# Optimization experiments

Measured on AMD Instinct MI355X. Metric: run time of the kernel, lower is better.

## Reference

```python
import jax, jax.numpy as jnp
import numpy as np

EMB_SCALE = 0.001  # embedding_scale when normalize=False


def setup_inputs() -> dict:
    key = jax.random.key(0)
    k1, k2 = jax.random.split(key)
    N, S, C, V, K = 8, 4096, 2, 128, 512
    x0 = jax.random.normal(k1, (N, S, C, V), dtype=jnp.float32)
    embedding = jax.random.normal(k2, (C, K, V), dtype=jnp.float32) * EMB_SCALE
    return {"x0": x0, "embedding": embedding}


def reference(x0, embedding):
    # normalize=False path: x = x0, embedding used as-is
    N, S, C, V = x0.shape
    K = embedding.shape[1]
    x = x0
    xf = x.reshape(N * S, C, V)  # (B, C, V), B = N*S tokens

    # (the ||x||^2 term is constant over k). Avoids materializing (B, C, K, V).
    dots = jnp.einsum('bcv,ckv->bck', xf, embedding)          # (B, C, K)
    e_sq = jnp.sum(embedding * embedding, axis=2)             # (C, K)
    dist2 = e_sq[None, :, :] - 2.0 * dots                     # (B, C, K)
    index = jnp.argmin(dist2, axis=2)                         # (B, C) int

    # Entropy of codebook usage (original divides by len(index) == B rows)
    B = N * S
    hist = jnp.bincount(index.reshape(-1), length=K).astype(jnp.float32)
    prob = hist / jnp.float32(B)
    entropy = -jnp.sum(jnp.where(hist > 0, prob * jnp.log(jnp.maximum(prob, 1e-30)), 0.0))

    # Gather: output[b, c] = embedding[c, index[b, c]]
    output = embedding[jnp.arange(C), index]                  # (B, C, V)
    output = output.reshape(N, S, C, V)

    out0 = jax.lax.stop_gradient(output - x) + x              # straight-through
    out1 = jnp.sum((jax.lax.stop_gradient(x) - output) ** 2, axis=3)  # (N,S,C)
    out2 = (jnp.sum((x - jax.lax.stop_gradient(output)) ** 2, axis=3)
            + jnp.sum((x - x0) ** 2, axis=3))                 # (N,S,C); (x-x0)==0 here
    return (out0, out1, out2, entropy)
```

## Files before the change

### kernel.cpp

```cpp
#include <hip/hip_runtime.h>
#include <math.h>

#define N_TOK    32768
#define C_CH     2
#define V_DIM    128
#define K_CODES  512
#define TPB      64
#define CAND_CAP 768
#define BAND     4.0e-3f

typedef short     bf16v8 __attribute__((ext_vector_type(8)));
typedef float     f32x4  __attribute__((ext_vector_type(4)));
typedef unsigned  u32x4  __attribute__((ext_vector_type(4)));

__device__ inline unsigned f2bf(float f) {
    unsigned u = __float_as_uint(f);
    return (u + 0x7FFFu + ((u >> 16) & 1u)) >> 16;
}
__device__ inline unsigned mapf(float d) {
    unsigned u = __float_as_uint(d);
    return ((int)u < 0) ? ~u : (u | 0x80000000u);
}
__device__ inline float unmapf(unsigned u) {
    return __uint_as_float((u & 0x80000000u) ? (u & 0x7FFFFFFFu) : ~u);
}

__global__ __launch_bounds__(64) void vq_prep(const float* __restrict__ emb,
                                              float* __restrict__ e_sq,
                                              unsigned int* __restrict__ hist,
                                              unsigned char* __restrict__ img) {
    const int row  = blockIdx.x;
    const int lane = threadIdx.x;
    const float a = emb[(size_t)row * V_DIM + lane];
    const float b = emb[(size_t)row * V_DIM + 64 + lane];
    float s = a * a + b * b;
#pragma unroll
    for (int off = 32; off; off >>= 1) s += __shfl_down(s, off);
    if (lane == 0) {
        e_sq[row] = s;
        if (row < K_CODES) hist[row] = 0u;
    }
    if (lane < 16) {
        const float* src = emb + (size_t)row * V_DIM + lane * 8;
        u32x4 val;
#pragma unroll
        for (int q = 0; q < 4; ++q)
            val[q] = f2bf(src[2 * q]) | (f2bf(src[2 * q + 1]) << 16);
        *reinterpret_cast<u32x4*>(img + ((size_t)row * 16 + lane) * 16) = val;
    }
}

__global__ __launch_bounds__(256, 2) void vq_main(const float* __restrict__ x0,
                                                  const float* __restrict__ emb,
                                                  const float* __restrict__ e_sq,
                                                  const unsigned char* __restrict__ img,
                                                  unsigned short* __restrict__ idx16,
                                                  float* __restrict__ out0,
                                                  float* __restrict__ out1,
                                                  float* __restrict__ out2) {
    __shared__ float xx_s[TPB];
    __shared__ unsigned int dmin_s[TPB];
    __shared__ unsigned long long best_s[TPB];
    __shared__ unsigned int cand[CAND_CAP];
    __shared__ int cand_n;

    const int c    = blockIdx.y;
    const int gt0  = blockIdx.x * TPB;
    const int t    = threadIdx.x;
    const int lane = t & 63;
    const int w    = t >> 6;
    const int l15  = lane & 15;
    const int l4   = lane >> 4;

    if (t < TPB) { dmin_s[t] = 0xFFFFFFFFu; best_s[t] = ~0ull; }
    if (t == 0) cand_n = 0;

    u32x4 Bf[8][4];
    {
        const unsigned char* imgc = img + (size_t)(c * K_CODES + w * 128) * 256;
#pragma unroll
        for (int ct = 0; ct < 8; ++ct)
#pragma unroll
            for (int kk = 0; kk < 4; ++kk)
                Bf[ct][kk] = *reinterpret_cast<const u32x4*>(
                    imgc + (size_t)(ct * 16 + l15) * 256 + (kk * 4 + l4) * 16);
    }
    float esq_r[8];
#pragma unroll
    for (int ct = 0; ct < 8; ++ct)
        esq_r[ct] = e_sq[c * K_CODES + w * 128 + ct * 16 + l15];

    __syncthreads();

    f32x4 raw[8];
    auto LOADX = [&](int tile_) {
        const float* xp = x0 + ((size_t)(gt0 + tile_ * 16 + l15) * C_CH + c) * V_DIM
                        + l4 * 8;
#pragma unroll
        for (int kk = 0; kk < 4; ++kk) {
            raw[2 * kk]     = *reinterpret_cast<const f32x4*>(xp + kk * 32);
            raw[2 * kk + 1] = *reinterpret_cast<const f32x4*>(xp + kk * 32 + 4);
        }
    };

    LOADX(0);
#pragma unroll
    for (int tile = 0; tile < 4; ++tile) {
        u32x4 A[4];
        float part = 0.f;
#pragma unroll
        for (int kk = 0; kk < 4; ++kk) {
            const f32x4 lo = raw[2 * kk], hi = raw[2 * kk + 1];
            u32x4 v;
            v[0] = f2bf(lo[0]) | (f2bf(lo[1]) << 16);
            v[1] = f2bf(lo[2]) | (f2bf(lo[3]) << 16);
            v[2] = f2bf(hi[0]) | (f2bf(hi[1]) << 16);
            v[3] = f2bf(hi[2]) | (f2bf(hi[3]) << 16);
            A[kk] = v;
#pragma unroll
            for (int z = 0; z < 4; ++z) {
                part = fmaf(lo[z], lo[z], part);
                part = fmaf(hi[z], hi[z], part);
            }
        }
        part += __shfl_xor(part, 16);
        part += __shfl_xor(part, 32);
        if (w == 0 && l4 == 0) xx_s[tile * 16 + l15] = part;

        if (tile < 3) LOADX(tile + 1);

        f32x4 acc[8];
#pragma unroll
        for (int ct = 0; ct < 8; ++ct) acc[ct] = (f32x4){0.f, 0.f, 0.f, 0.f};
#pragma unroll
        for (int kk = 0; kk < 4; ++kk)
#pragma unroll
            for (int ct = 0; ct < 8; ++ct)
                acc[ct] = __builtin_amdgcn_mfma_f32_16x16x32_bf16(
                    __builtin_bit_cast(bf16v8, A[kk]),
                    __builtin_bit_cast(bf16v8, Bf[ct][kk]), acc[ct], 0, 0, 0);

#pragma unroll
        for (int ct = 0; ct < 8; ++ct)
#pragma unroll
            for (int r = 0; r < 4; ++r)
                acc[ct][r] = fmaf(-2.f, acc[ct][r], esq_r[ct]);
#pragma unroll
        for (int r = 0; r < 4; ++r) {
            float v = acc[0][r];
#pragma unroll
            for (int ct = 1; ct < 8; ++ct) v = fminf(v, acc[ct][r]);
#pragma unroll
            for (int s = 1; s < 16; s <<= 1) v = fminf(v, __shfl_xor(v, s));
            if (l15 == 0)
                atomicMin(&dmin_s[tile * 16 + l4 * 4 + r], mapf(v));
        }
        __syncthreads();

#pragma unroll
        for (int r = 0; r < 4; ++r) {
            const int tok = tile * 16 + l4 * 4 + r;
            const float thr = unmapf(dmin_s[tok]) + BAND;
#pragma unroll
            for (int ct = 0; ct < 8; ++ct) {
                if (acc[ct][r] <= thr) {
                    const int k = w * 128 + ct * 16 + l15;
                    const int pos = atomicAdd(&cand_n, 1);
                    if (pos < CAND_CAP)
                        cand[pos] = ((unsigned)tok << 9) | (unsigned)k;
                }
            }
        }
    }
    __syncthreads();

    {
        const int nc = cand_n < CAND_CAP ? cand_n : CAND_CAP;
        const int g  = t >> 4;
        const int gl = t & 15;
        for (int i = g; i < nc; i += 16) {
            const unsigned key = cand[i];
            const int tok = key >> 9;
            const int kc  = key & (K_CODES - 1);
            const float* xg = x0 + ((size_t)(gt0 + tok) * C_CH + c) * V_DIM + gl * 8;
            const float* eg = emb + ((size_t)c * K_CODES + kc) * V_DIM + gl * 8;
            const f32x4 xa = *reinterpret_cast<const f32x4*>(xg);
            const f32x4 xb = *reinterpret_cast<const f32x4*>(xg + 4);
            const f32x4 ea = *reinterpret_cast<const f32x4*>(eg);
            const f32x4 eb = *reinterpret_cast<const f32x4*>(eg + 4);
            float d8 = 0.f;
#pragma unroll
            for (int z = 0; z < 4; ++z) {
                d8 = fmaf(xa[z], ea[z], d8);
                d8 = fmaf(xb[z], eb[z], d8);
            }
#pragma unroll
            for (int s = 1; s < 16; s <<= 1) d8 += __shfl_xor(d8, s);
            if (gl == 0) {
                const float d = fmaf(-2.f, d8, e_sq[c * K_CODES + kc]);
                atomicMin(&best_s[tok],
                          ((unsigned long long)mapf(d) << 32) | (unsigned)kc);
            }
        }
    }
    __syncthreads();

    if (t < TPB) {
        const unsigned long long b = best_s[t];
        const int k = (int)(b & (unsigned)(K_CODES - 1));
        const float d = unmapf((unsigned)(b >> 32));
        const float o12 = xx_s[t] + d;
        const size_t oi = (size_t)(gt0 + t) * C_CH + c;
        out1[oi] = o12;
        out2[oi] = o12;
        idx16[oi] = (unsigned short)k;
    }

#pragma unroll
    for (int p = 0; p < 8; ++p) {
        const int tok = p * 8 + (t >> 5);
        const int v4  = t & 31;
        const int k   = (int)(best_s[tok] & (unsigned long long)(K_CODES - 1));
        const f32x4 ev = *reinterpret_cast<const f32x4*>(
            emb + ((size_t)c * K_CODES + k) * V_DIM + v4 * 4);
        const f32x4 xv = *reinterpret_cast<const f32x4*>(
            x0 + ((size_t)(gt0 + tok) * C_CH + c) * V_DIM + v4 * 4);
        f32x4 ov;
#pragma unroll
        for (int z = 0; z < 4; ++z) ov[z] = (ev[z] - xv[z]) + xv[z];
        *reinterpret_cast<f32x4*>(
            out0 + ((size_t)(gt0 + tok) * C_CH + c) * V_DIM + v4 * 4) = ov;
    }
}

__global__ __launch_bounds__(256) void vq_hist(const unsigned short* __restrict__ idx16,
                                               unsigned int* __restrict__ hist) {
    __shared__ unsigned int h[K_CODES];
    const int t = threadIdx.x;
    h[t] = 0u; h[t + 256] = 0u;
    __syncthreads();
    const int base = blockIdx.x * 4096;
#pragma unroll
    for (int j = 0; j < 16; ++j)
        atomicAdd(&h[idx16[base + j * 256 + t]], 1u);
    __syncthreads();
    if (h[t])       atomicAdd(&hist[t],       h[t]);
    if (h[t + 256]) atomicAdd(&hist[t + 256], h[t + 256]);
}

__global__ __launch_bounds__(512) void vq_entropy(const unsigned int* __restrict__ hist,
                                                  float* __restrict__ ent) {
    const int t = threadIdx.x;
    float v = 0.f;
    const unsigned int h = hist[t];
    if (h > 0u) {
        const float p = (float)h * (1.0f / 32768.0f);
        v = p * logf(p);
    }
#pragma unroll
    for (int off = 32; off; off >>= 1) v += __shfl_down(v, off);
    __shared__ float s[8];
    if ((t & 63) == 0) s[t >> 6] = v;
    __syncthreads();
    if (t == 0) {
        float tot = 0.f;
#pragma unroll
        for (int i = 0; i < 8; ++i) tot += s[i];
        ent[0] = -tot;
    }
}

extern "C" void kernel_launch(void* const* d_in, const int* in_sizes, int n_in,
                              void* d_out, int out_size, void* d_ws, size_t ws_size,
                              hipStream_t stream) {
    const float* x0  = (const float*)d_in[0];
    const float* emb = (const float*)d_in[1];

    float*          e_sq  = (float*)d_ws;
    unsigned int*   hist  = (unsigned int*)((char*)d_ws + 4096);
    unsigned char*  img   = (unsigned char*)d_ws + 8192;
    unsigned short* idx16 = (unsigned short*)((char*)d_ws + 8192 + 262144);

    float* out0 = (float*)d_out;
    float* out1 = out0 + (size_t)N_TOK * C_CH * V_DIM;
    float* out2 = out1 + (size_t)N_TOK * C_CH;
    float* ent  = out2 + (size_t)N_TOK * C_CH;

    vq_prep<<<C_CH * K_CODES, 64, 0, stream>>>(emb, e_sq, hist, img);
    vq_main<<<dim3(N_TOK / TPB, C_CH), 256, 0, stream>>>(x0, emb, e_sq, img, idx16,
                                                         out0, out1, out2);
    vq_hist<<<16, 256, 0, stream>>>(idx16, hist);
    vq_entropy<<<1, K_CODES, 0, stream>>>(hist, ent);
}
```

Baseline: 76.64 us.

## Use per-wave candidate lists without block barriers and fuse histogram into main kernel

Candidate refinement moves from one block-wide shared list to four per-wave lists (128 entries each). Each wave now rescores only its own candidates, so the two __syncthreads in the distance phase are removed. The threshold is then read from a partially reduced per-token minimum, which is looser and lets more candidates through; with the smaller per-wave cap, overflow could drop the true best code. The separate histogram kernel and the idx16 buffer are removed: each token's chosen code is added straight into the global histogram with an atomic, which saves a launch but adds contended global atomics.

```diff
diff --git a/kernel.cpp b/kernel.cpp
--- a/kernel.cpp
+++ b/kernel.cpp
@@ -6,7 +6,7 @@
 #define V_DIM    128
 #define K_CODES  512
 #define TPB      64
-#define CAND_CAP 768
+#define WCAP     128
 #define BAND     4.0e-3f
 
 typedef short     bf16v8 __attribute__((ext_vector_type(8)));
@@ -54,15 +54,15 @@
                                                   const float* __restrict__ emb,
                                                   const float* __restrict__ e_sq,
                                                   const unsigned char* __restrict__ img,
-                                                  unsigned short* __restrict__ idx16,
+                                                  unsigned int* __restrict__ hist,
                                                   float* __restrict__ out0,
                                                   float* __restrict__ out1,
                                                   float* __restrict__ out2) {
     __shared__ float xx_s[TPB];
     __shared__ unsigned int dmin_s[TPB];
     __shared__ unsigned long long best_s[TPB];
-    __shared__ unsigned int cand[CAND_CAP];
-    __shared__ int cand_n;
+    __shared__ unsigned int cand_w[4][WCAP];
+    __shared__ int cnt_w[4];
 
     const int c    = blockIdx.y;
     const int gt0  = blockIdx.x * TPB;
@@ -73,7 +73,7 @@
     const int l4   = lane >> 4;
 
     if (t < TPB) { dmin_s[t] = 0xFFFFFFFFu; best_s[t] = ~0ull; }
-    if (t == 0) cand_n = 0;
+    if (t < 4) cnt_w[t] = 0;
 
     u32x4 Bf[8][4];
     {
@@ -145,6 +145,7 @@
 #pragma unroll
             for (int r = 0; r < 4; ++r)
                 acc[ct][r] = fmaf(-2.f, acc[ct][r], esq_r[ct]);
+
 #pragma unroll
         for (int r = 0; r < 4; ++r) {
             float v = acc[0][r];
@@ -155,7 +156,6 @@
             if (l15 == 0)
                 atomicMin(&dmin_s[tile * 16 + l4 * 4 + r], mapf(v));
         }
-        __syncthreads();
 
 #pragma unroll
         for (int r = 0; r < 4; ++r) {
@@ -165,25 +165,23 @@
             for (int ct = 0; ct < 8; ++ct) {
                 if (acc[ct][r] <= thr) {
                     const int k = w * 128 + ct * 16 + l15;
-                    const int pos = atomicAdd(&cand_n, 1);
-                    if (pos < CAND_CAP)
-                        cand[pos] = ((unsigned)tok << 9) | (unsigned)k;
+                    const int pos = atomicAdd(&cnt_w[w], 1);
+                    if (pos < WCAP)
+                        cand_w[w][pos] = ((unsigned)tok << 9) | (unsigned)k;
                 }
             }
         }
     }
-    __syncthreads();
 
     {
-        const int nc = cand_n < CAND_CAP ? cand_n : CAND_CAP;
-        const int g  = t >> 4;
-        const int gl = t & 15;
-        for (int i = g; i < nc; i += 16) {
-            const unsigned key = cand[i];
+        const int cnt0 = cnt_w[w];
+        const int cnt  = cnt0 < WCAP ? cnt0 : WCAP;
+        for (int i = l4; i < cnt; i += 4) {
+            const unsigned key = cand_w[w][i];
             const int tok = key >> 9;
             const int kc  = key & (K_CODES - 1);
-            const float* xg = x0 + ((size_t)(gt0 + tok) * C_CH + c) * V_DIM + gl * 8;
-            const float* eg = emb + ((size_t)c * K_CODES + kc) * V_DIM + gl * 8;
+            const float* xg = x0 + ((size_t)(gt0 + tok) * C_CH + c) * V_DIM + l15 * 8;
+            const float* eg = emb + ((size_t)c * K_CODES + kc) * V_DIM + l15 * 8;
             const f32x4 xa = *reinterpret_cast<const f32x4*>(xg);
             const f32x4 xb = *reinterpret_cast<const f32x4*>(xg + 4);
             const f32x4 ea = *reinterpret_cast<const f32x4*>(eg);
@@ -196,7 +194,7 @@
             }
 #pragma unroll
             for (int s = 1; s < 16; s <<= 1) d8 += __shfl_xor(d8, s);
-            if (gl == 0) {
+            if (l15 == 0) {
                 const float d = fmaf(-2.f, d8, e_sq[c * K_CODES + kc]);
                 atomicMin(&best_s[tok],
                           ((unsigned long long)mapf(d) << 32) | (unsigned)kc);
@@ -213,7 +211,7 @@
         const size_t oi = (size_t)(gt0 + t) * C_CH + c;
         out1[oi] = o12;
         out2[oi] = o12;
-        idx16[oi] = (unsigned short)k;
+        atomicAdd(&hist[k], 1u);
     }
 
 #pragma unroll
@@ -233,21 +231,6 @@
     }
 }
 
-__global__ __launch_bounds__(256) void vq_hist(const unsigned short* __restrict__ idx16,
-                                               unsigned int* __restrict__ hist) {
-    __shared__ unsigned int h[K_CODES];
-    const int t = threadIdx.x;
-    h[t] = 0u; h[t + 256] = 0u;
-    __syncthreads();
-    const int base = blockIdx.x * 4096;
-#pragma unroll
-    for (int j = 0; j < 16; ++j)
-        atomicAdd(&h[idx16[base + j * 256 + t]], 1u);
-    __syncthreads();
-    if (h[t])       atomicAdd(&hist[t],       h[t]);
-    if (h[t + 256]) atomicAdd(&hist[t + 256], h[t + 256]);
-}
-
 __global__ __launch_bounds__(512) void vq_entropy(const unsigned int* __restrict__ hist,
                                                   float* __restrict__ ent) {
     const int t = threadIdx.x;
@@ -276,10 +259,9 @@
     const float* x0  = (const float*)d_in[0];
     const float* emb = (const float*)d_in[1];
 
-    float*          e_sq  = (float*)d_ws;
-    unsigned int*   hist  = (unsigned int*)((char*)d_ws + 4096);
-    unsigned char*  img   = (unsigned char*)d_ws + 8192;
-    unsigned short* idx16 = (unsigned short*)((char*)d_ws + 8192 + 262144);
+    float*         e_sq = (float*)d_ws;
+    unsigned int*  hist = (unsigned int*)((char*)d_ws + 4096);
+    unsigned char* img  = (unsigned char*)d_ws + 8192;
 
     float* out0 = (float*)d_out;
     float* out1 = out0 + (size_t)N_TOK * C_CH * V_DIM;
@@ -287,8 +269,7 @@
     float* ent  = out2 + (size_t)N_TOK * C_CH;
 
     vq_prep<<<C_CH * K_CODES, 64, 0, stream>>>(emb, e_sq, hist, img);
-    vq_main<<<dim3(N_TOK / TPB, C_CH), 256, 0, stream>>>(x0, emb, e_sq, img, idx16,
+    vq_main<<<dim3(N_TOK / TPB, C_CH), 256, 0, stream>>>(x0, emb, e_sq, img, hist,
                                                          out0, out1, out2);
-    vq_hist<<<16, 256, 0, stream>>>(idx16, hist);
     vq_entropy<<<1, K_CODES, 0, stream>>>(hist, ent);
 }
```

Measured after the change: 76.49 us. About the same (-0.2%).
